# Optimization experiments

Measured on AMD Instinct MI355X. Metric: run time of the kernel, lower is better.

## Reference

```python
import jax, jax.numpy as jnp
import numpy as np

NEGPOS_RATIO = 3


def _smooth_l1(pred, tgt):
    d = jnp.abs(pred - tgt)
    return jnp.where(d < 1.0, 0.5 * d * d, d - 0.5)


def setup_inputs() -> dict:
    key = jax.random.key(0)
    B, P, C = 64, 8732, 81
    ks = jax.random.split(key, 7)
    loc_dataT = jax.random.normal(ks[0], (B, P, 4), jnp.float32)
    conf_dataT = jax.random.normal(ks[1], (B, P, C), jnp.float32)
    loc_dataS = jax.random.normal(ks[2], (B, P, 4), jnp.float32)
    conf_dataS = jax.random.normal(ks[3], (B, P, C), jnp.float32)
    loc_t = jax.random.normal(ks[4], (B, P, 4), jnp.float32)
    is_pos = jax.random.uniform(ks[5], (B, P)) < 0.02
    labels = jax.random.randint(ks[6], (B, P), 1, C, dtype=jnp.int32)
    conf_t = jnp.where(is_pos, labels, 0).astype(jnp.int32)
    return {
        "loc_dataT": loc_dataT, "conf_dataT": conf_dataT,
        "loc_dataS": loc_dataS, "conf_dataS": conf_dataS,
        "loc_t": loc_t, "conf_t": conf_t,
    }


def _multibox_losses(loc_dataT, conf_dataT, loc_dataS, conf_dataS, loc_t, conf_t):
    B, P, C = conf_dataT.shape
    pos = conf_t > 0                                    # [B,P]
    posf = pos.astype(conf_dataT.dtype)

    # Localization SmoothL1 over positive priors (reduction='sum')
    loss_lT = jnp.sum(_smooth_l1(loc_dataT, loc_t) * posf[..., None])
    loss_lS = jnp.sum(_smooth_l1(loc_dataS, loc_t) * posf[..., None])

    # Per-prior CE loss: logsumexp(conf) - conf[gt]  (== -log_softmax[gt])
    def per_prior_ce(conf):
        lse = jax.nn.logsumexp(conf, axis=-1)           # [B,P]
        gt = jnp.take_along_axis(conf, conf_t[..., None].astype(jnp.int32), axis=-1)[..., 0]
        return lse - gt

    lcT = per_prior_ce(conf_dataT)                      # [B,P]
    lcS = per_prior_ce(conf_dataS)

    # Hard negative mining: rank negatives by loss (positives zeroed first)
    def neg_mask(lc, num_neg):
        lc_m = jnp.where(pos, 0.0, lc)
        order = jnp.argsort(-lc_m, axis=1)              # descending sort indices
        rank = jnp.argsort(order, axis=1)               # rank of each prior
        return rank < num_neg

    num_pos = jnp.sum(pos.astype(jnp.int32), axis=1, keepdims=True)   # [B,1]
    num_neg = jnp.minimum(NEGPOS_RATIO * num_pos, P - 1)
    negT = neg_mask(lcT, num_neg)
    negS = neg_mask(lcS, num_neg)

    # Confidence CE over positives + mined negatives (reduction='sum')
    loss_cT = jnp.sum(jnp.where(pos | negT, lcT, 0.0))
    loss_cS = jnp.sum(jnp.where(pos | negS, lcS, 0.0))

    N = jnp.sum(num_pos).astype(conf_dataT.dtype)
    return jnp.stack([loss_lT / N, loss_cT / N, loss_lS / N, loss_cS / N])


def reference(loc_dataT, conf_dataT, loc_dataS, conf_dataS, loc_t, conf_t):
    # Teacher branch is detached in the original module.
    loc_dataT = jax.lax.stop_gradient(loc_dataT)
    conf_dataT = jax.lax.stop_gradient(conf_dataT)
    return _multibox_losses(loc_dataT, conf_dataT, loc_dataS, conf_dataS, loc_t, conf_t)
```

## Files before the change

kernel.cpp:

```cpp
#include <hip/hip_runtime.h>

#define BB 64
#define PP 8732
#define CC 81


__device__ __forceinline__ float sl1(float d) {
    d = fabsf(d);
    return d < 1.0f ? 0.5f * d * d : d - 0.5f;
}

__device__ __forceinline__ float blockReduceF(float v, volatile float* sb) {
    for (int off = 32; off; off >>= 1) v += __shfl_xor(v, off, 64);
    __syncthreads();
    if ((threadIdx.x & 63) == 0) sb[threadIdx.x >> 6] = v;
    __syncthreads();
    float r = 0.0f;
    int nw = blockDim.x >> 6;
    for (int i = 0; i < nw; ++i) r += sb[i];
    return r;
}

__device__ __forceinline__ int blockReduceI(int v, volatile int* sb) {
    for (int off = 32; off; off >>= 1) v += __shfl_xor(v, off, 64);
    __syncthreads();
    if ((threadIdx.x & 63) == 0) sb[threadIdx.x >> 6] = v;
    __syncthreads();
    int r = 0;
    int nw = blockDim.x >> 6;
    for (int i = 0; i < nw; ++i) r += sb[i];
    return r;
}

__global__ void kInit(float* acc, int* numpos, int* ctr, float* locPart) {
    int t = threadIdx.x;
    if (t < 4) acc[t] = 0.0f;
    if (t < BB) { numpos[t] = 0; locPart[t] = 0.0f; locPart[BB + t] = 0.0f; }
    if (t == 0) ctr[0] = 0;
}

__device__ __forceinline__ float rowSumExp(const float* __restrict__ conf,
                                           size_t f0, int d) {
    const float4* __restrict__ p = (const float4*)(conf + (f0 - (size_t)d));
    float4 v0 = p[0];
    float a0 = (d <= 0) ? __expf(v0.x) : 0.0f;
    float a1 = (d <= 1) ? __expf(v0.y) : 0.0f;
    float a2 = (d <= 2) ? __expf(v0.z) : 0.0f;
    float a3 = __expf(v0.w);
    #pragma unroll
    for (int k = 1; k < 20; ++k) {
        float4 v = p[k];
        a0 += __expf(v.x);
        a1 += __expf(v.y);
        a2 += __expf(v.z);
        a3 += __expf(v.w);
    }
    float4 vl = p[20];
    a0 += __expf(vl.x);
    a1 += (d >= 1) ? __expf(vl.y) : 0.0f;
    a2 += (d >= 2) ? __expf(vl.z) : 0.0f;
    a3 += (d >= 3) ? __expf(vl.w) : 0.0f;
    return (a0 + a1) + (a2 + a3);
}

__global__ __launch_bounds__(256, 8) void kStream(
        const float* __restrict__ confT, const float* __restrict__ confS,
        const int* __restrict__ conft,
        const float4* __restrict__ locT4, const float4* __restrict__ locS4,
        const float4* __restrict__ loct4,
        float* __restrict__ lcT, float* __restrict__ lcS,
        float* __restrict__ locPart, int* __restrict__ numpos) {
    int b = blockIdx.y;
    int p = blockIdx.x * 256 + threadIdx.x;
    int lane = threadIdx.x & 63;

    float sT = 0.0f, sS = 0.0f;
    int cnt = 0;

    if (p < PP) {
        size_t gr = (size_t)b * PP + p;
        int g = conft[gr];
        size_t f0 = gr * (size_t)CC;
        int d = (int)(f0 & 3);

        float sumT = rowSumExp(confT, f0, d);
        float sumS = rowSumExp(confS, f0, d);

        float gtT = confT[f0 + (size_t)g];
        float gtS = confS[f0 + (size_t)g];

        float lcTv = __logf(sumT) - gtT;
        float lcSv = __logf(sumS) - gtS;
        bool pos = g > 0;
        lcT[gr] = pos ? -(lcTv + 1.0f) : lcTv;
        lcS[gr] = pos ? -(lcSv + 1.0f) : lcSv;

        if (pos) {
            float4 gt = loct4[gr];
            float4 aT = locT4[gr];
            float4 aS = locS4[gr];
            sT = sl1(aT.x - gt.x) + sl1(aT.y - gt.y) + sl1(aT.z - gt.z) + sl1(aT.w - gt.w);
            sS = sl1(aS.x - gt.x) + sl1(aS.y - gt.y) + sl1(aS.z - gt.z) + sl1(aS.w - gt.w);
            cnt = 1;
        }
    }

    for (int off = 32; off; off >>= 1) {
        sT  += __shfl_xor(sT,  off, 64);
        sS  += __shfl_xor(sS,  off, 64);
        cnt += __shfl_xor(cnt, off, 64);
    }
    if (lane == 0 && cnt) {
        atomicAdd(&locPart[b], sT);
        atomicAdd(&locPart[BB + b], sS);
        atomicAdd(&numpos[b], cnt);
    }
}

#define WROT(w, bin) (((w) << 8) | (((bin) + (w) * 17) & 0xFF))
__global__ __launch_bounds__(1024) void kC(const float* __restrict__ lcT,
                                           const float* __restrict__ lcS,
                                           const int* __restrict__ numpos,
                                           const float* __restrict__ locPart,
                                           float* acc, int* ctr,
                                           float* __restrict__ out) {
    __shared__ unsigned keys[PP];
    __shared__ int whist[16 * 256];
    __shared__ int hist[256];
    __shared__ float fsb[16];
    __shared__ int isb[16];
    __shared__ int selBin, selAbove, lastFlag, wsum[4];
    int b = blockIdx.y;
    int tid = threadIdx.x;
    int lane = tid & 63;
    const float* src = ((blockIdx.x == 0) ? lcT : lcS) + (size_t)b * PP;

    float posSum = 0.0f;
    for (int i = tid; i < PP; i += 1024) {
        float v = src[i];
        keys[i] = (v < 0.0f) ? 0u : __float_as_uint(v);
        if (v < 0.0f) posSum += (-v - 1.0f);
    }
    posSum = blockReduceF(posSum, fsb);

    int np = numpos[b];
    int k = min(3 * np, PP - 1);
    float mined = 0.0f;
    if (k > 0) {
        unsigned prefix = 0;
        int kk = k;
        int wid = tid >> 6;
        for (int round = 0; round < 4; ++round) {
            int shift = 24 - 8 * round;
            for (int i = tid; i < 16 * 256; i += 1024) whist[i] = 0;
            __syncthreads();
            for (int i = tid; i < PP; i += 1024) {
                unsigned key = keys[i];
                bool match = (round == 0) || ((key >> (shift + 8)) == prefix);
                if (match) atomicAdd(&whist[WROT(wid, (key >> shift) & 0xFF)], 1);
            }
            __syncthreads();
            if (tid < 256) {
                int h2 = 0;
                #pragma unroll
                for (int w = 0; w < 16; ++w) h2 += whist[WROT(w, tid)];
                hist[tid] = h2;
            }
            __syncthreads();
            int x = (tid < 256) ? hist[tid] : 0;
            for (int d = 1; d < 64; d <<= 1) {
                int y = __shfl_down(x, d, 64);
                if (lane + d < 64) x += y;
            }
            if (tid < 256 && lane == 0) wsum[tid >> 6] = x;
            __syncthreads();
            if (tid < 256) {
                int wv = tid >> 6;
                int add = 0;
                if (wv < 3) add += wsum[wv + 1];
                if (wv < 2) add += wsum[wv + 2];
                if (wv < 1) add += wsum[wv + 3];
                int sfx = x + add;
                hist[tid] = sfx;
            }
            __syncthreads();
            if (tid < 256) {
                int above = (tid < 255) ? hist[tid + 1] : 0;
                if (above < kk && hist[tid] >= kk) {
                    selBin = tid;
                    selAbove = above;
                }
            }
            __syncthreads();
            prefix = (prefix << 8) | (unsigned)selBin;
            kk -= selAbove;
            __syncthreads();
        }
        int c = 0;
        float s = 0.0f;
        for (int i = tid; i < PP; i += 1024) {
            unsigned key = keys[i];
            if (key > prefix) { c += 1; s += __uint_as_float(key); }
        }
        c = blockReduceI(c, isb);
        s = blockReduceF(s, fsb);
        mined = s + (float)(k - c) * __uint_as_float(prefix);
    }
    if (tid == 0) {
        atomicAdd(&acc[(blockIdx.x == 0) ? 2 : 3], posSum + mined);
        __threadfence();
        int old = atomicAdd(ctr, 1);
        lastFlag = (old == 2 * BB - 1) ? 1 : 0;
    }
    __syncthreads();
    if (lastFlag) {
        __threadfence();
        int v = 0;
        float pT = 0.0f, pS = 0.0f;
        if (tid < BB) {
            v  = __hip_atomic_load(&numpos[tid], __ATOMIC_RELAXED, __HIP_MEMORY_SCOPE_AGENT);
            pT = __hip_atomic_load(&locPart[tid], __ATOMIC_RELAXED, __HIP_MEMORY_SCOPE_AGENT);
            pS = __hip_atomic_load(&locPart[BB + tid], __ATOMIC_RELAXED, __HIP_MEMORY_SCOPE_AGENT);
        }
        if (tid < 64) {
            for (int off = 32; off; off >>= 1) {
                v  += __shfl_xor(v,  off, 64);
                pT += __shfl_xor(pT, off, 64);
                pS += __shfl_xor(pS, off, 64);
            }
        }
        if (tid == 0) {
            float N = (float)v;
            float a2 = __hip_atomic_load(&acc[2], __ATOMIC_RELAXED, __HIP_MEMORY_SCOPE_AGENT);
            float a3 = __hip_atomic_load(&acc[3], __ATOMIC_RELAXED, __HIP_MEMORY_SCOPE_AGENT);
            out[0] = pT / N;
            out[1] = a2 / N;
            out[2] = pS / N;
            out[3] = a3 / N;
        }
    }
}

extern "C" void kernel_launch(void* const* d_in, const int* in_sizes, int n_in,
                              void* d_out, int out_size, void* d_ws, size_t ws_size,
                              hipStream_t stream) {
    const float* locT  = (const float*)d_in[0];
    const float* confT = (const float*)d_in[1];
    const float* locS  = (const float*)d_in[2];
    const float* confS = (const float*)d_in[3];
    const float* loct  = (const float*)d_in[4];
    const int*   conft = (const int*)d_in[5];
    float* out = (float*)d_out;

    float* lcT = (float*)d_ws;
    float* lcS = lcT + (size_t)BB * PP;
    float* acc = lcS + (size_t)BB * PP;
    int* numpos = (int*)(acc + 4);
    int* ctr = numpos + BB;
    float* locPart = (float*)(ctr + 1);

    kInit<<<1, 64, 0, stream>>>(acc, numpos, ctr, locPart);

    dim3 gS((PP + 255) / 256, BB);
    kStream<<<gS, 256, 0, stream>>>(confT, confS, conft,
                                    (const float4*)locT, (const float4*)locS,
                                    (const float4*)loct, lcT, lcS,
                                    locPart, numpos);

    dim3 gC(2, BB);
    kC<<<gC, 1024, 0, stream>>>(lcT, lcS, numpos, locPart, acc, ctr, out);
}
```

Measured before the change: 499.4 us.

## Split each confidence row across four lanes for coalesced float4 loads

The streaming kernel now assigns four lanes to each prior row instead of one thread per row. Each lane reads interleaved float4 chunks of the 81-class row, and partial exp sums are combined with shuffles. The goal is to coalesce the global loads, which were previously strided by row length per thread, and to increase memory-level parallelism. The cost is that each block covers four times fewer priors and needs extra shuffles, plus clamped reads for out-of-range rows.

New measurement: 428.0 us. 1.17x faster.

```diff
diff --git a/kernel.cpp b/kernel.cpp
--- a/kernel.cpp
+++ b/kernel.cpp
@@ -39,27 +39,26 @@
     if (t == 0) ctr[0] = 0;
 }
 
-__device__ __forceinline__ float rowSumExp(const float* __restrict__ conf,
-                                           size_t f0, int d) {
-    const float4* __restrict__ p = (const float4*)(conf + (f0 - (size_t)d));
-    float4 v0 = p[0];
-    float a0 = (d <= 0) ? __expf(v0.x) : 0.0f;
-    float a1 = (d <= 1) ? __expf(v0.y) : 0.0f;
-    float a2 = (d <= 2) ? __expf(v0.z) : 0.0f;
+__device__ __forceinline__ float qRowSumExp(const float4* __restrict__ p,
+                                            int h, int dd, int d) {
+    float4 v0 = p[h];
+    float a0 = (dd <= 0) ? __expf(v0.x) : 0.0f;
+    float a1 = (dd <= 1) ? __expf(v0.y) : 0.0f;
+    float a2 = (dd <= 2) ? __expf(v0.z) : 0.0f;
     float a3 = __expf(v0.w);
     #pragma unroll
-    for (int k = 1; k < 20; ++k) {
-        float4 v = p[k];
-        a0 += __expf(v.x);
-        a1 += __expf(v.y);
-        a2 += __expf(v.z);
-        a3 += __expf(v.w);
-    }
-    float4 vl = p[20];
-    a0 += __expf(vl.x);
-    a1 += (d >= 1) ? __expf(vl.y) : 0.0f;
-    a2 += (d >= 2) ? __expf(vl.z) : 0.0f;
-    a3 += (d >= 3) ? __expf(vl.w) : 0.0f;
+    for (int k = 1; k < 5; ++k) {
+        float4 v = p[h + 4 * k];
+        a0 += __expf(v.x); a1 += __expf(v.y);
+        a2 += __expf(v.z); a3 += __expf(v.w);
+    }
+    if (h == 0) {
+        float4 vl = p[20];
+        a0 += __expf(vl.x);
+        a1 += (d >= 1) ? __expf(vl.y) : 0.0f;
+        a2 += (d >= 2) ? __expf(vl.z) : 0.0f;
+        a3 += (d >= 3) ? __expf(vl.w) : 0.0f;
+    }
     return (a0 + a1) + (a2 + a3);
 }
 
@@ -71,30 +70,52 @@
         float* __restrict__ lcT, float* __restrict__ lcS,
         float* __restrict__ locPart, int* __restrict__ numpos) {
     int b = blockIdx.y;
-    int p = blockIdx.x * 256 + threadIdx.x;
-    int lane = threadIdx.x & 63;
+    int tid = threadIdx.x;
+    int lane = tid & 63;
+    int w = tid >> 6;
+    int h = lane & 3;
+    int r = lane >> 2;
+    int p0 = blockIdx.x * 64 + w * 16;
+    int prow = p0 + r;
+    bool valid = prow < PP;
+    int pclamp = valid ? prow : PP - 1;
+
+    int g16 = 0;
+    {
+        int pr = p0 + lane;
+        int prc = (pr < PP) ? pr : PP - 1;
+        if (lane < 16) g16 = conft[(size_t)b * PP + prc];
+    }
+    int gv = __shfl(g16, r, 64);
+
+    size_t gr = (size_t)b * PP + (size_t)pclamp;
+    size_t f0 = gr * (size_t)CC;
+    int d = (int)(f0 & 3);
+    size_t q0 = (f0 - (size_t)d) >> 2;
+
+    float gtT = 0.0f, gtS = 0.0f;
+    if (h == 0) {
+        gtT = confT[f0 + (size_t)gv];
+        gtS = confS[f0 + (size_t)gv];
+    }
+
+    int dd = (h == 0) ? d : 0;
+    float sumT = qRowSumExp((const float4*)confT + q0, h, dd, d);
+    float sumS = qRowSumExp((const float4*)confS + q0, h, dd, d);
+
+    sumT += __shfl_xor(sumT, 1, 64);
+    sumT += __shfl_xor(sumT, 2, 64);
+    sumS += __shfl_xor(sumS, 1, 64);
+    sumS += __shfl_xor(sumS, 2, 64);
 
     float sT = 0.0f, sS = 0.0f;
     int cnt = 0;
-
-    if (p < PP) {
-        size_t gr = (size_t)b * PP + p;
-        int g = conft[gr];
-        size_t f0 = gr * (size_t)CC;
-        int d = (int)(f0 & 3);
-
-        float sumT = rowSumExp(confT, f0, d);
-        float sumS = rowSumExp(confS, f0, d);
-
-        float gtT = confT[f0 + (size_t)g];
-        float gtS = confS[f0 + (size_t)g];
-
+    bool pos = gv > 0;
+    if (h == 0 && valid) {
         float lcTv = __logf(sumT) - gtT;
         float lcSv = __logf(sumS) - gtS;
-        bool pos = g > 0;
         lcT[gr] = pos ? -(lcTv + 1.0f) : lcTv;
         lcS[gr] = pos ? -(lcSv + 1.0f) : lcSv;
-
         if (pos) {
             float4 gt = loct4[gr];
             float4 aT = locT4[gr];
@@ -261,7 +282,7 @@
 
     kInit<<<1, 64, 0, stream>>>(acc, numpos, ctr, locPart);
 
-    dim3 gS((PP + 255) / 256, BB);
+    dim3 gS((PP + 63) / 64, BB);
     kStream<<<gS, 256, 0, stream>>>(confT, confS, conft,
                                     (const float4*)locT, (const float4*)locS,
                                     (const float4*)loct, lcT, lcS,
```
